# Performance work log

Measured on AMD Instinct MI355X. Metric: run time of the kernel, lower is better.

## Reference

```python
import jax, jax.numpy as jnp
import numpy as np

B, T, F, H = 64, 256, 64, 512  # batch, seq_len, temporal_feature_num, hidden_size_lstm


def setup_inputs() -> dict:
    key = jax.random.key(0)
    ks = jax.random.split(key, 8)
    return {
        "temporal_features": jax.random.normal(ks[0], (B, T, F), dtype=jnp.float32),
        "temporal_masks": jax.random.uniform(ks[1], (B, T, F), dtype=jnp.float32),
        "h0": jax.random.normal(ks[2], (F, B, H), dtype=jnp.float32),
        "c0": jax.random.normal(ks[3], (F, B, H), dtype=jnp.float32),
        "W_ih": jax.random.normal(ks[4], (F, 4 * H, 2), dtype=jnp.float32) * 0.05,
        "W_hh": jax.random.normal(ks[5], (F, 4 * H, H), dtype=jnp.float32) * 0.05,
        "b_ih": jax.random.normal(ks[6], (F, 4 * H), dtype=jnp.float32) * 0.05,
        "b_hh": jax.random.normal(ks[7], (F, 4 * H), dtype=jnp.float32) * 0.05,
    }


def reference(temporal_features, temporal_masks, h0, c0, W_ih, W_hh, b_ih, b_hh):
    # x: [T, F, B, 2] -- per feature, the LSTM input is (feature_value, mask)
    x = jnp.stack([temporal_features, temporal_masks], axis=-1)  # [B, T, F, 2]
    x = jnp.transpose(x, (1, 2, 0, 3))  # [T, F, B, 2]

    bias = (b_ih + b_hh)[:, None, :]  # [F, 1, 4H]

    def step(carry, x_t):
        h, c = carry  # each [F, B, H]
        gates = (jnp.einsum('fbi,fgi->fbg', x_t, W_ih)
                 + jnp.einsum('fbh,fgh->fbg', h, W_hh)
                 + bias)  # [F, B, 4H]
        i_g, f_g, g_g, o_g = jnp.split(gates, 4, axis=-1)  # torch LSTMCell gate order i,f,g,o
        i_g = jax.nn.sigmoid(i_g)
        f_g = jax.nn.sigmoid(f_g)
        g_g = jnp.tanh(g_g)
        o_g = jax.nn.sigmoid(o_g)
        c_new = f_g * c + i_g * g_g
        h_new = o_g * jnp.tanh(c_new)
        return (h_new, c_new), None

    (h_final, _), _ = jax.lax.scan(step, (h0, c0), x)
    return h_final  # [F, B, H] -- stacked version of the returned h_list
```

## Files before the change

kernel.cpp:

```cpp
#include <hip/hip_runtime.h>
#include <hip/hip_bf16.h>
#include <stdint.h>

#define F_N 64
#define T_N 256
#define B_N 64
#define H_N 512
#define STREAM_KS 10
#define VREG_KS0 10
#define LDS_KS0 14

typedef __attribute__((ext_vector_type(8))) __bf16 bf16x8;
typedef __attribute__((ext_vector_type(4))) float f32x4;
typedef __attribute__((ext_vector_type(4))) uint32_t u32x4;


__global__ void pack_x_kernel(const float* __restrict__ tf, const float* __restrict__ tm,
                              float* __restrict__ xp) {
  int tid = blockIdx.x * 256 + threadIdx.x;
  if (tid >= T_N * B_N * F_N) return;
  int f = tid & 63;
  int b = (tid >> 6) & 63;
  int t = tid >> 12;
  float v = tf[((size_t)b * T_N + t) * F_N + f];
  float m = tm[((size_t)b * T_N + t) * F_N + f];
  float* dst = xp + (((size_t)t * F_N + f) * B_N + b) * 2;
  dst[0] = v;
  dst[1] = m;
}

__global__ void pack_h0_kernel(const float* __restrict__ h0, __bf16* __restrict__ hx0) {
  int tid = blockIdx.x * 256 + threadIdx.x;
  if (tid < F_N * B_N * H_N) hx0[tid] = (__bf16)h0[tid];
}

__global__ void pack_w_kernel(const float* __restrict__ Whh, __bf16* __restrict__ Wp) {
  int gtid = blockIdx.x * 256 + threadIdx.x;
  int lane = gtid & 63;
  int nt = (gtid >> 6) & 3;
  int ks = (gtid >> 8) & 15;
  int w = (gtid >> 12) & 7;
  int q = (gtid >> 15) & 3;
  int f = gtid >> 17;
  int l15 = lane & 15, lhi = lane >> 4;
  int n_local = w * 64 + nt * 16 + l15;
  int r_local = n_local >> 2;
  int gam = n_local & 3;
  int grow = gam * 512 + q * 128 + r_local;
  const float* src = Whh + ((size_t)f * 2048 + grow) * 512 + ks * 32 + lhi * 8;
  float4 u0 = *(const float4*)src;
  float4 u1 = *(const float4*)(src + 4);
  bf16x8 v;
  v[0] = (__bf16)u0.x; v[1] = (__bf16)u0.y; v[2] = (__bf16)u0.z; v[3] = (__bf16)u0.w;
  v[4] = (__bf16)u1.x; v[5] = (__bf16)u1.y; v[6] = (__bf16)u1.z; v[7] = (__bf16)u1.w;
  *(bf16x8*)((char*)Wp + (size_t)gtid * 16) = v;
}


__global__ void __launch_bounds__(512, 1) __attribute__((amdgpu_waves_per_eu(2, 2)))
lstm_main(
    const float* __restrict__ c0, const __bf16* __restrict__ Wp,
    const float* __restrict__ Wih, const float* __restrict__ bih,
    const float* __restrict__ bhh, const float* __restrict__ xp,
    __bf16* hx, unsigned int* barr, unsigned int* xcdmap, float* __restrict__ out) {
  const int blk = blockIdx.x;
  const int f = blk & 63;
  const int q = blk >> 6;
  const int tid = threadIdx.x;
  const int lane = tid & 63;
  const int w = tid >> 6;
  const int l15 = lane & 15;
  const int lhi = lane >> 4;
  const int ls = lane & 3;
  const int lr = l15 >> 2;

  __shared__ __align__(16) unsigned char lds_h[65536];
  __shared__ __align__(16) unsigned char lds_stage[16384];
  __shared__ __align__(16) unsigned char lds_wst[65536];
  __shared__ __align__(16) float ldsB[512];
  __shared__ __align__(16) float lds0[512];
  __shared__ __align__(16) float lds1[512];
  __shared__ int s_same;

  {
    int i = tid;
    int r = i >> 2, g = i & 3;
    int row = g * 512 + q * 128 + r;
    size_t ro = (size_t)f * 2048 + row;
    ldsB[i] = bih[ro] + bhh[ro];
    lds0[i] = Wih[ro * 2 + 0];
    lds1[i] = Wih[ro * 2 + 1];
  }

  if (tid == 0) {
    uint32_t xcc;
    asm volatile("s_getreg_b32 %0, hwreg(HW_REG_XCC_ID)" : "=s"(xcc));
    xcc &= 15u;
    __hip_atomic_store(&xcdmap[f * 4 + q], xcc + 1u, __ATOMIC_RELAXED,
                       __HIP_MEMORY_SCOPE_AGENT);
    uint32_t ids[4];
    int ok = 1;
    for (int j = 0; j < 4; ++j) {
      unsigned int it = 0;
      uint32_t v;
      do {
        v = __hip_atomic_load(&xcdmap[f * 4 + j], __ATOMIC_RELAXED,
                              __HIP_MEMORY_SCOPE_AGENT);
        if (++it > 2000000u) { ok = 0; break; }
        if (v == 0u) __builtin_amdgcn_s_sleep(2);
      } while (v == 0u);
      ids[j] = v;
    }
    if (ok) ok = (ids[0] == ids[1]) & (ids[1] == ids[2]) & (ids[2] == ids[3]);
    s_same = ok;
  }

  const bf16x8* wpbase = (const bf16x8*)Wp + ((size_t)((f * 4 + q) * 8 + w)) * 4096 + lane;

  bf16x8 s[3][4];
#define LOAD_SLOT(SL, KS)                                       \
  {                                                             \
    _Pragma("unroll") for (int nt_ = 0; nt_ < 4; ++nt_)         \
        s[SL][nt_] = wpbase[((KS) * 4 + nt_) * 64];             \
  }

  bf16x8 wsf[4][4];
#pragma unroll
  for (int s2 = 0; s2 < 4; ++s2)
#pragma unroll
    for (int nt = 0; nt < 4; ++nt) wsf[s2][nt] = wpbase[((VREG_KS0 + s2) * 4 + nt) * 64];

#pragma unroll
  for (int ksi = 0; ksi < 2; ++ksi)
#pragma unroll
    for (int nt = 0; nt < 4; ++nt) {
      bf16x8 v = wpbase[((LDS_KS0 + ksi) * 4 + nt) * 64];
      *(bf16x8*)(lds_wst + (((ksi * 8 + w) * 4 + nt) << 10) + lane * 16) = v;
    }

  float c_reg[4][4];
#pragma unroll
  for (int mt = 0; mt < 4; ++mt) {
    int brow = mt * 16 + lhi * 4 + ls;
#pragma unroll
    for (int nt = 0; nt < 4; ++nt) {
      int rg = w * 16 + nt * 4 + lr;
      c_reg[mt][nt] = c0[((size_t)f * B_N + brow) * H_N + q * 128 + rg];
    }
  }

  const size_t hxfeat = (size_t)f * (B_N * H_N);
  const size_t hxstride = (size_t)F_N * B_N * H_N;

  {
    const unsigned char* src = (const unsigned char*)(hx + hxfeat);
    uint32_t b = tid >> 3;
    uint32_t off = (tid & 7) * 32;
    uint32_t sw = (b & 7) << 4;
#pragma unroll
    for (int qq = 0; qq < 4; ++qq) {
      uint32_t gb = b * 1024 + qq * 256 + off;
      uint4 u0 = *(const uint4*)(src + gb);
      uint4 u1 = *(const uint4*)(src + gb + 16);
      *(uint4*)(lds_h + (gb ^ sw)) = u0;
      *(uint4*)(lds_h + ((gb + 16) ^ sw)) = u1;
    }
  }
  LOAD_SLOT(0, 0);
  LOAD_SLOT(1, 1);
  LOAD_SLOT(2, 2);
  __syncthreads();
  const bool fastpath = (s_same != 0);

#define READ_A(KS)                                                                     \
  {                                                                                    \
    _Pragma("unroll") for (int mt = 0; mt < 4; ++mt) {                                 \
      int row = mt * 16 + l15;                                                         \
      uint32_t byteoff =                                                               \
          (uint32_t)(row * 1024) + (((uint32_t)((KS) * 64 + lhi * 16)) ^ ((row & 7) << 4)); \
      a[mt] = *(const bf16x8*)(lds_h + byteoff);                                       \
    }                                                                                  \
  }
#define MFMA_W(WARR)                                                                   \
  {                                                                                    \
    _Pragma("unroll") for (int mt = 0; mt < 4; ++mt)                                   \
        _Pragma("unroll") for (int nt = 0; nt < 4; ++nt)                               \
            acc[mt][nt] = __builtin_amdgcn_mfma_f32_16x16x32_bf16(a[mt], (WARR)[nt],   \
                                                                  acc[mt][nt], 0, 0, 0); \
  }
#define STATIC_V(S2) { READ_A(VREG_KS0 + (S2)); MFMA_W(wsf[S2]); }
#define STATIC_L(KSI)                                                                  \
  {                                                                                    \
    READ_A(LDS_KS0 + (KSI));                                                           \
    bf16x8 wfrag[4];                                                                   \
    _Pragma("unroll") for (int nt = 0; nt < 4; ++nt) wfrag[nt] =                       \
        *(const bf16x8*)(lds_wst + ((((KSI) * 8 + w) * 4 + nt) << 10) + lane * 16);    \
    MFMA_W(wfrag);                                                                     \
  }
#define STREAM(KS)                                                                     \
  {                                                                                    \
    READ_A(KS);                                                                        \
    MFMA_W(s[(KS) % 3]);                                                               \
    if ((KS) + 3 < STREAM_KS) {                                                        \
      _Pragma("unroll") for (int nt_ = 0; nt_ < 4; ++nt_)                              \
          s[(KS) % 3][nt_] = wpbase[(((KS) + 3) * 4 + nt_) * 64];                      \
    }                                                                                  \
  }

#pragma unroll 1
  for (int t = 0; t < T_N; ++t) {
    f32x4 acc[4][4] = {};
    bf16x8 a[4];

    STATIC_V(0); STREAM(0);
    STATIC_V(1); STREAM(1);
    STATIC_V(2); STREAM(2);
    STATIC_V(3); STREAM(3);
    STATIC_L(0); STREAM(4);
    STATIC_L(1); STREAM(5);
    STREAM(6); STREAM(7); STREAM(8); STREAM(9);

    const bool last = (t == T_N - 1);
    const float* xpt = xp + (((size_t)t * F_N + f) * B_N) * 2;
#pragma unroll
    for (int mt = 0; mt < 4; ++mt) {
      int brow = mt * 16 + lhi * 4 + ls;
      float xv = xpt[brow * 2];
      float xm = xpt[brow * 2 + 1];
#pragma unroll
      for (int nt = 0; nt < 4; ++nt) {
        float v0 = acc[mt][nt][0], v1 = acc[mt][nt][1], v2 = acc[mt][nt][2], v3 = acc[mt][nt][3];
        {
          float t0 = __shfl_xor(v0, 1), t1 = __shfl_xor(v1, 1),
                t2 = __shfl_xor(v2, 1), t3 = __shfl_xor(v3, 1);
          if (lane & 1) { v0 = t1; v2 = t3; } else { v1 = t0; v3 = t2; }
        }
        {
          float t0 = __shfl_xor(v0, 2), t1 = __shfl_xor(v1, 2),
                t2 = __shfl_xor(v2, 2), t3 = __shfl_xor(v3, 2);
          if (lane & 2) { v0 = t2; v1 = t3; } else { v2 = t0; v3 = t1; }
        }
        int rg = w * 16 + nt * 4 + lr;
        int idx4 = rg << 2;
        float4 tb = *(const float4*)&ldsB[idx4];
        float4 w0t = *(const float4*)&lds0[idx4];
        float4 w1t = *(const float4*)&lds1[idx4];
        v0 += tb.x + w0t.x * xv + w1t.x * xm;
        v1 += tb.y + w0t.y * xv + w1t.y * xm;
        v2 += tb.z + w0t.z * xv + w1t.z * xm;
        v3 += tb.w + w0t.w * xv + w1t.w * xm;
        float ig = __builtin_amdgcn_rcpf(1.0f + __expf(-v0));
        float fg = __builtin_amdgcn_rcpf(1.0f + __expf(-v1));
        float gg = 2.0f * __builtin_amdgcn_rcpf(1.0f + __expf(-2.0f * v2)) - 1.0f;
        float og = __builtin_amdgcn_rcpf(1.0f + __expf(-v3));
        float cn = fg * c_reg[mt][nt] + ig * gg;
        c_reg[mt][nt] = cn;
        float th = 2.0f * __builtin_amdgcn_rcpf(1.0f + __expf(-2.0f * cn)) - 1.0f;
        float hn = og * th;
        if (last) {
          out[((size_t)f * B_N + brow) * H_N + q * 128 + rg] = hn;
        } else {
          uint32_t sw = (uint32_t)((brow & 7) << 4);
          *(__bf16*)(lds_stage + ((uint32_t)(brow * 256 + rg * 2) ^ sw)) = (__bf16)hn;
        }
      }
    }
    if (last) break;

    __syncthreads();

    {
      __bf16* dstbuf = hx + ((size_t)((t + 1) & 1)) * hxstride + hxfeat;
      uint32_t b = tid >> 3;
      uint32_t off = (tid & 7) * 32;
      uint32_t sw = (b & 7) << 4;
      u32x4 u0 = *(const u32x4*)(lds_stage + ((b * 256 + off) ^ sw));
      u32x4 u1 = *(const u32x4*)(lds_stage + ((b * 256 + off + 16) ^ sw));
      unsigned char* dp = (unsigned char*)dstbuf + b * 1024 + q * 256 + off;
      if (fastpath) {
        asm volatile("global_store_dwordx4 %0, %1, off sc0" ::"v"(dp), "v"(u0) : "memory");
        asm volatile("global_store_dwordx4 %0, %1, off sc0" ::"v"(dp + 16), "v"(u1) : "memory");
        asm volatile("s_waitcnt vmcnt(0)" ::: "memory");
      } else {
        *(u32x4*)(dp) = u0;
        *(u32x4*)(dp + 16) = u1;
      }
      uint32_t hb = b * 1024 + q * 256 + off;
      *(u32x4*)(lds_h + (hb ^ sw)) = u0;
      *(u32x4*)(lds_h + ((hb + 16) ^ sw)) = u1;
    }
    __syncthreads();

    if (tid == 0) {
      unsigned int* bp = barr + f * T_N + t;
      if (fastpath)
        __hip_atomic_fetch_add(bp, 1u, __ATOMIC_RELAXED, __HIP_MEMORY_SCOPE_AGENT);
      else
        __hip_atomic_fetch_add(bp, 1u, __ATOMIC_RELEASE, __HIP_MEMORY_SCOPE_AGENT);
    }
    LOAD_SLOT(0, 0);
    LOAD_SLOT(1, 1);
    LOAD_SLOT(2, 2);
    if (tid == 0) {
      unsigned int* bp = barr + f * T_N + t;
      unsigned int it = 0;
      while (__hip_atomic_load(bp, __ATOMIC_RELAXED, __HIP_MEMORY_SCOPE_AGENT) < 4u) {
        __builtin_amdgcn_s_sleep(1);
        if (++it > 4000000u) break;
      }
      if (!fastpath)
        (void)__hip_atomic_load(bp, __ATOMIC_ACQUIRE, __HIP_MEMORY_SCOPE_AGENT);
    }
    __syncthreads();

    if (fastpath) {
      asm volatile("buffer_inv sc0" ::: "memory");
    }
    {
      const unsigned char* src =
          (const unsigned char*)(hx + ((size_t)((t + 1) & 1)) * hxstride + hxfeat);
      uint32_t b = tid >> 3;
      uint32_t off = (tid & 7) * 32;
      uint32_t sw = (b & 7) << 4;
#pragma unroll
      for (int qq = 0; qq < 4; ++qq) {
        if (qq == q) continue;
        uint32_t gb = b * 1024 + qq * 256 + off;
        uint4 u0 = *(const uint4*)(src + gb);
        uint4 u1 = *(const uint4*)(src + gb + 16);
        *(uint4*)(lds_h + (gb ^ sw)) = u0;
        *(uint4*)(lds_h + ((gb + 16) ^ sw)) = u1;
      }
    }
    __syncthreads();
  }
#undef LOAD_SLOT
#undef READ_A
#undef MFMA_W
#undef STATIC_V
#undef STATIC_L
#undef STREAM
}

extern "C" void kernel_launch(void* const* d_in, const int* in_sizes, int n_in,
                              void* d_out, int out_size, void* d_ws, size_t ws_size,
                              hipStream_t stream) {
  const float* tf = (const float*)d_in[0];
  const float* tm = (const float*)d_in[1];
  const float* h0 = (const float*)d_in[2];
  const float* c0 = (const float*)d_in[3];
  const float* Wih = (const float*)d_in[4];
  const float* Whh = (const float*)d_in[5];
  const float* bih = (const float*)d_in[6];
  const float* bhh = (const float*)d_in[7];
  float* out = (float*)d_out;

  const size_t WP_BYTES = (size_t)8388608 * 16;
  const size_t XP_BYTES = (size_t)T_N * F_N * B_N * 2 * 4;
  const size_t HX_BYTES = (size_t)2 * F_N * B_N * H_N * 2;
  const size_t BARR_BYTES = (size_t)F_N * T_N * 4;
  const size_t MAP_BYTES = 1024;
  if (ws_size < WP_BYTES + XP_BYTES + HX_BYTES + BARR_BYTES + MAP_BYTES) return;

  char* ws = (char*)d_ws;
  __bf16* Wp = (__bf16*)ws;
  float* xp = (float*)(ws + WP_BYTES);
  __bf16* hx = (__bf16*)(ws + WP_BYTES + XP_BYTES);
  unsigned int* barr = (unsigned int*)(ws + WP_BYTES + XP_BYTES + HX_BYTES);
  unsigned int* xcdmap = (unsigned int*)(ws + WP_BYTES + XP_BYTES + HX_BYTES + BARR_BYTES);

  hipMemsetAsync(barr, 0, BARR_BYTES + MAP_BYTES, stream);
  pack_x_kernel<<<(T_N * B_N * F_N + 255) / 256, 256, 0, stream>>>(tf, tm, xp);
  pack_h0_kernel<<<(F_N * B_N * H_N + 255) / 256, 256, 0, stream>>>(h0, hx);
  pack_w_kernel<<<8388608 / 256, 256, 0, stream>>>(Whh, Wp);
  lstm_main<<<256, 512, 0, stream>>>(c0, Wp, Wih, bih, bhh, xp, hx, barr, xcdmap, out);
}
```

Measured before the change: 7.390 ms.

## Stream recurrent weights via async global-to-LDS DMA double buffer

```diff
diff --git a/kernel.cpp b/kernel.cpp
--- a/kernel.cpp
+++ b/kernel.cpp
@@ -8,11 +8,17 @@
 #define H_N 512
 #define STREAM_KS 10
 #define VREG_KS0 10
-#define LDS_KS0 14
+#define NVSTAT 6
 
 typedef __attribute__((ext_vector_type(8))) __bf16 bf16x8;
 typedef __attribute__((ext_vector_type(4))) float f32x4;
 typedef __attribute__((ext_vector_type(4))) uint32_t u32x4;
+
+__device__ __forceinline__ void dma16(const void* g, void* l) {
+  __builtin_amdgcn_global_load_lds(
+      (const __attribute__((address_space(1))) void*)g,
+      (__attribute__((address_space(3))) void*)l, 16, 0, 0);
+}
 
 
 __global__ void pack_x_kernel(const float* __restrict__ tf, const float* __restrict__ tm,
@@ -76,7 +82,7 @@
 
   __shared__ __align__(16) unsigned char lds_h[65536];
   __shared__ __align__(16) unsigned char lds_stage[16384];
-  __shared__ __align__(16) unsigned char lds_wst[65536];
+  __shared__ __align__(16) unsigned char lds_ws[65536];
   __shared__ __align__(16) float ldsB[512];
   __shared__ __align__(16) float lds0[512];
   __shared__ __align__(16) float lds1[512];
@@ -116,27 +122,21 @@
   }
 
   const bf16x8* wpbase = (const bf16x8*)Wp + ((size_t)((f * 4 + q) * 8 + w)) * 4096 + lane;
-
-  bf16x8 s[3][4];
-#define LOAD_SLOT(SL, KS)                                       \
-  {                                                             \
-    _Pragma("unroll") for (int nt_ = 0; nt_ < 4; ++nt_)         \
-        s[SL][nt_] = wpbase[((KS) * 4 + nt_) * 64];             \
-  }
-
-  bf16x8 wsf[4][4];
-#pragma unroll
-  for (int s2 = 0; s2 < 4; ++s2)
+  const char* wgb = (const char*)Wp +
+                    (((size_t)((f * 4 + q) * 8 + w)) * 4096 + (size_t)lane) * 16;
+
+#define ISSUE_KS(KS2)                                                                  \
+  {                                                                                    \
+    _Pragma("unroll") for (int ni_ = 0; ni_ < 4; ++ni_)                                \
+        dma16(wgb + ((((KS2)) * 4 + ni_) << 10),                                       \
+              lds_ws + ((((KS2)) & 1) * 32768 + (w << 12) + (ni_ << 10)));             \
+  }
+
+  bf16x8 wsf[NVSTAT][4];
+#pragma unroll
+  for (int s2 = 0; s2 < NVSTAT; ++s2)
 #pragma unroll
     for (int nt = 0; nt < 4; ++nt) wsf[s2][nt] = wpbase[((VREG_KS0 + s2) * 4 + nt) * 64];
-
-#pragma unroll
-  for (int ksi = 0; ksi < 2; ++ksi)
-#pragma unroll
-    for (int nt = 0; nt < 4; ++nt) {
-      bf16x8 v = wpbase[((LDS_KS0 + ksi) * 4 + nt) * 64];
-      *(bf16x8*)(lds_wst + (((ksi * 8 + w) * 4 + nt) << 10) + lane * 16) = v;
-    }
 
   float c_reg[4][4];
 #pragma unroll
@@ -166,9 +166,8 @@
       *(uint4*)(lds_h + ((gb + 16) ^ sw)) = u1;
     }
   }
-  LOAD_SLOT(0, 0);
-  LOAD_SLOT(1, 1);
-  LOAD_SLOT(2, 2);
+  ISSUE_KS(0);
+  ISSUE_KS(1);
   __syncthreads();
   const bool fastpath = (s_same != 0);
 
@@ -189,22 +188,21 @@
                                                                   acc[mt][nt], 0, 0, 0); \
   }
 #define STATIC_V(S2) { READ_A(VREG_KS0 + (S2)); MFMA_W(wsf[S2]); }
-#define STATIC_L(KSI)                                                                  \
-  {                                                                                    \
-    READ_A(LDS_KS0 + (KSI));                                                           \
-    bf16x8 wfrag[4];                                                                   \
-    _Pragma("unroll") for (int nt = 0; nt < 4; ++nt) wfrag[nt] =                       \
-        *(const bf16x8*)(lds_wst + ((((KSI) * 8 + w) * 4 + nt) << 10) + lane * 16);    \
-    MFMA_W(wfrag);                                                                     \
-  }
 #define STREAM(KS)                                                                     \
   {                                                                                    \
     READ_A(KS);                                                                        \
-    MFMA_W(s[(KS) % 3]);                                                               \
-    if ((KS) + 3 < STREAM_KS) {                                                        \
-      _Pragma("unroll") for (int nt_ = 0; nt_ < 4; ++nt_)                              \
-          s[(KS) % 3][nt_] = wpbase[(((KS) + 3) * 4 + nt_) * 64];                      \
+    asm volatile("s_waitcnt vmcnt(%0)" ::"i"(((KS) == STREAM_KS - 1) ? 0 : 4)          \
+                 : "memory");                                                          \
+    bf16x8 wfrag[4];                                                                   \
+    _Pragma("unroll") for (int nt_ = 0; nt_ < 4; ++nt_) wfrag[nt_] =                   \
+        *(const bf16x8*)(lds_ws + (((KS) & 1) * 32768 + (w << 12) + (nt_ << 10)) +     \
+                         (lane << 4));                                                 \
+    asm volatile("s_waitcnt lgkmcnt(0)" ::: "memory");                                 \
+    if ((KS) + 2 < STREAM_KS) {                                                        \
+      ISSUE_KS((KS) + 2);                                                              \
+      __builtin_amdgcn_sched_barrier(0);                                               \
     }                                                                                  \
+    MFMA_W(wfrag);                                                                     \
   }
 
 #pragma unroll 1
@@ -212,13 +210,14 @@
     f32x4 acc[4][4] = {};
     bf16x8 a[4];
 
-    STATIC_V(0); STREAM(0);
-    STATIC_V(1); STREAM(1);
-    STATIC_V(2); STREAM(2);
-    STATIC_V(3); STREAM(3);
-    STATIC_L(0); STREAM(4);
-    STATIC_L(1); STREAM(5);
-    STREAM(6); STREAM(7); STREAM(8); STREAM(9);
+    STREAM(0); STREAM(1);
+    STATIC_V(0); STREAM(2);
+    STATIC_V(1); STREAM(3);
+    STATIC_V(2); STREAM(4);
+    STATIC_V(3); STREAM(5);
+    STATIC_V(4); STREAM(6);
+    STATIC_V(5); STREAM(7);
+    STREAM(8); STREAM(9);
 
     const bool last = (t == T_N - 1);
     const float* xpt = xp + (((size_t)t * F_N + f) * B_N) * 2;
@@ -298,9 +297,8 @@
       else
         __hip_atomic_fetch_add(bp, 1u, __ATOMIC_RELEASE, __HIP_MEMORY_SCOPE_AGENT);
     }
-    LOAD_SLOT(0, 0);
-    LOAD_SLOT(1, 1);
-    LOAD_SLOT(2, 2);
+    ISSUE_KS(0);
+    ISSUE_KS(1);
     if (tid == 0) {
       unsigned int* bp = barr + f * T_N + t;
       unsigned int it = 0;
@@ -334,11 +332,10 @@
     }
     __syncthreads();
   }
-#undef LOAD_SLOT
+#undef ISSUE_KS
 #undef READ_A
 #undef MFMA_W
 #undef STATIC_V
-#undef STATIC_L
 #undef STREAM
 }
 
```

Result: slower. 9.833 ms (+33.0%).
